# Optimization experiments

Hardware: AMD Instinct MI355X
Metric: run time of the kernel (lower is better)

The kernel has to match this reference:

```python
import jax, jax.numpy as jnp
import numpy as np

NUM_CLASSES = 10
NPTS = 100            # quadrature points per unit interval (torch default npts=100)
EPS = 1e-5            # self.epsilon in the torch module
BATCH = 131072
C_IN = 512


def _betaln(a, b):
    return jax.lax.lgamma(a) + jax.lax.lgamma(b) - jax.lax.lgamma(a + b)


def setup_inputs() -> dict:
    key = jax.random.key(0)
    k1, k2, k3, k4, k5 = jax.random.split(key, 5)
    s = 1.0 / np.sqrt(C_IN).astype(np.float32)
    x = jax.random.normal(k1, (BATCH, C_IN), dtype=jnp.float32)
    W_alpha = jax.random.normal(k2, (C_IN, 1), dtype=jnp.float32) * s
    b_alpha = jax.random.normal(k3, (1,), dtype=jnp.float32) * s
    W_beta = jax.random.normal(k4, (C_IN, 1), dtype=jnp.float32) * s
    b_beta = jax.random.normal(k5, (1,), dtype=jnp.float32) * s
    return {"x": x, "W_alpha": W_alpha, "b_alpha": b_alpha,
            "W_beta": W_beta, "b_beta": b_beta}


def reference(x, W_alpha, b_alpha, W_beta, b_beta):
    # alpha, beta: [B, 1], clamp(1 + softplus(linear(x)), 1, 100)
    alpha = jnp.clip(1.0 + jax.nn.softplus(x @ W_alpha + b_alpha), 1.0, 100.0)
    beta = jnp.clip(1.0 + jax.nn.softplus(x @ W_beta + b_beta), 1.0, 100.0)
    lbeta = _betaln(alpha, beta)  # [B, 1] log Beta-function normalizer
    dx = 1.0 / (NPTS * NUM_CLASSES)

    def unnorm_cdf(b_thr):
        # torch: linspace(eps, b-eps, int(npts*b)); Beta.log_prob broadcast [B, n]
        n = int(NPTS * b_thr)
        if n == 0:
            return jnp.zeros((x.shape[0],), dtype=x.dtype)
        grid = jnp.linspace(EPS, b_thr - EPS, n, dtype=x.dtype)  # [n]
        logpdf = ((alpha - 1.0) * jnp.log(grid)
                  + (beta - 1.0) * jnp.log1p(-grid)
                  - lbeta)  # [B, n]
        return jnp.exp(logpdf).sum(axis=1) * dx  # [B]

    # thresholds i/C for i = 0..C (static Python loop over C+1 small fixed set)
    cdfs = [unnorm_cdf(i / NUM_CLASSES) for i in range(NUM_CLASSES + 1)]
    probs = jnp.stack([cdfs[i + 1] - cdfs[i] for i in range(NUM_CLASSES)], axis=1)  # [B, C]
    # torch uses diag(1/rowsum) @ probs == row-broadcast normalization
    return probs / probs.sum(axis=1, keepdims=True)
```

## Files before the change

### kernel.cpp

```cpp
#include <hip/hip_runtime.h>
#include <math.h>

#define EPS_F 1e-5f
#define NPOINTS 550
#define CIN 512

static __device__ __forceinline__ float softplus_f(float z) {
    return fmaxf(z, 0.0f) + log1pf(expf(-fabsf(z)));
}

static __device__ __forceinline__ float dot8(const float4 a0, const float4 a1,
                                             const float4 w0, const float4 w1) {
    float s = a0.x * w0.x;
    s = fmaf(a0.y, w0.y, s);
    s = fmaf(a0.z, w0.z, s);
    s = fmaf(a0.w, w0.w, s);
    s = fmaf(a1.x, w1.x, s);
    s = fmaf(a1.y, w1.y, s);
    s = fmaf(a1.z, w1.z, s);
    s = fmaf(a1.w, w1.w, s);
    return s;
}

__global__ __launch_bounds__(256, 4) void beta_unimodal_kernel(
    const float* __restrict__ x,
    const float* __restrict__ Wa, const float* __restrict__ ba,
    const float* __restrict__ Wb, const float* __restrict__ bb,
    float* __restrict__ out)
{
    __shared__ float2 tab[NPOINTS];
    __shared__ float outbuf[32 * 10];
    __shared__ float part[4][2][8][68];

    const int tid = threadIdx.x;

    for (int p = tid; p < NPOINTS; p += 256) {
        int i = 1, off = 0;
        while (p >= off + 10 * i) { off += 10 * i; ++i; }
        const int j = p - off;
        const int n = 10 * i;
        const float thr = (float)i * 0.1f;
        const float step = (thr - 2.0f * EPS_F) / (float)(n - 1);
        const float g = EPS_F + step * (float)j;
        float2 e;
        e.x = log2f(g);
        e.y = log2f(1.0f - g);
        tab[p] = e;
    }
    __syncthreads();

    const int lane = tid & 63;
    const int wave = tid >> 6;
    const long rowBase = (long)blockIdx.x * 32 + wave * 8;

    const float4* Wa4 = (const float4*)Wa;
    const float4* Wb4 = (const float4*)Wb;
    const float4 wa0 = Wa4[lane], wa1 = Wa4[64 + lane];
    const float4 wb0 = Wb4[lane], wb1 = Wb4[64 + lane];

    float pa[8], pb[8];
    #pragma unroll
    for (int r = 0; r < 8; ++r) {
        const float4* xr = (const float4*)(x + (rowBase + r) * CIN);
        const float4 x0 = xr[lane];
        const float4 x1 = xr[64 + lane];
        pa[r] = dot8(x0, x1, wa0, wa1);
        pb[r] = dot8(x0, x1, wb0, wb1);
    }

    #pragma unroll
    for (int r = 0; r < 8; ++r) {
        part[wave][0][r][lane] = pa[r];
        part[wave][1][r][lane] = pb[r];
    }
    asm volatile("s_waitcnt lgkmcnt(0)" ::: "memory");

    const int row = lane >> 3;
    const int o = lane & 7;
    const int v = o >> 2;
    const int qa = o & 3;
    const float2* src2 = (const float2*)&part[wave][v][row][qa * 16];
    float s = 0.0f;
    #pragma unroll
    for (int c = 0; c < 8; ++c) {
        const float2 t = src2[c];
        s += t.x + t.y;
    }
    s += __shfl_xor(s, 1, 64);
    s += __shfl_xor(s, 2, 64);
    const float other = __shfl_xor(s, 4, 64);
    const float my_da = (v == 0) ? s : other;
    const float my_db = (v == 0) ? other : s;

    const float za = my_da + ba[0];
    const float zb = my_db + bb[0];
    const float alpha = fminf(fmaxf(1.0f + softplus_f(za), 1.0f), 100.0f);
    const float beta  = fminf(fmaxf(1.0f + softplus_f(zb), 1.0f), 100.0f);
    const float am1 = alpha - 1.0f;
    const float bm1 = beta - 1.0f;

    const float denom = am1 + bm1;
    float mode = (denom > 0.0f) ? (am1 / denom) : 0.5f;
    mode = fminf(fmaxf(mode, 1e-7f), 1.0f - 1.1920929e-7f);
    const float M2 = am1 * log2f(mode) + bm1 * log2f(1.0f - mode);

    float seg[10];
    int p0 = 0;
    #pragma unroll
    for (int i = 1; i <= 10; ++i) {
        const int n = 10 * i;
        float s2 = 0.0f;
        for (int j = o; j < n; j += 8) {
            const float2 t = tab[p0 + j];
            const float e = fmaf(am1, t.x, bm1 * t.y) - M2;
            s2 += __builtin_amdgcn_exp2f(e);
        }
        s2 += __shfl_xor(s2, 1, 64);
        s2 += __shfl_xor(s2, 2, 64);
        s2 += __shfl_xor(s2, 4, 64);
        seg[i - 1] = s2;
        p0 += n;
    }

    const float inv = 1.0f / seg[9];
    const int rowLocal = wave * 8 + row;
    {
        const float prev = (o > 0) ? seg[o - 1] : 0.0f;
        outbuf[rowLocal * 10 + o] = (seg[o] - prev) * inv;
        if (o < 2) {
            const int k = o + 8;
            outbuf[rowLocal * 10 + k] = (seg[k] - seg[k - 1]) * inv;
        }
    }
    __syncthreads();

    if (tid < 80) {
        const float4* src = (const float4*)outbuf;
        float4* dst = (float4*)(out + (size_t)blockIdx.x * 320);
        dst[tid] = src[tid];
    }
}

extern "C" void kernel_launch(void* const* d_in, const int* in_sizes, int n_in,
                              void* d_out, int out_size, void* d_ws, size_t ws_size,
                              hipStream_t stream) {
    const float* x  = (const float*)d_in[0];
    const float* Wa = (const float*)d_in[1];
    const float* ba = (const float*)d_in[2];
    const float* Wb = (const float*)d_in[3];
    const float* bb = (const float*)d_in[4];
    float* out = (float*)d_out;

    const int batch = in_sizes[0] / CIN;
    const int blocks = batch / 32;
    beta_unimodal_kernel<<<blocks, 256, 0, stream>>>(x, Wa, ba, Wb, bb, out);
}
```

Before: 362.3 us.

## Process 64 rows per wave with double-buffered x loads across iterations

Each wave now loops over eight 8-row chunks and prefetches the next chunk of x into registers while computing the current one. The goal is to hide global-load latency and to amortise the per-block log-table setup and weight loads over eight times more rows. The table sum now reads two grid points per float4 from LDS, and outputs are written straight to global memory instead of being staged through shared memory. In exchange, register pressure rises (launch bounds drop to 2 blocks per SIMD), the grid shrinks eightfold, and output stores become less coalesced.

```diff
diff --git a/kernel.cpp b/kernel.cpp
--- a/kernel.cpp
+++ b/kernel.cpp
@@ -4,6 +4,7 @@
 #define EPS_F 1e-5f
 #define NPOINTS 550
 #define CIN 512
+#define NITER 8
 
 static __device__ __forceinline__ float softplus_f(float z) {
     return fmaxf(z, 0.0f) + log1pf(expf(-fabsf(z)));
@@ -22,17 +23,32 @@
     return s;
 }
 
-__global__ __launch_bounds__(256, 4) void beta_unimodal_kernel(
+__global__ __launch_bounds__(256, 2) void beta_unimodal_kernel(
     const float* __restrict__ x,
     const float* __restrict__ Wa, const float* __restrict__ ba,
     const float* __restrict__ Wb, const float* __restrict__ bb,
     float* __restrict__ out)
 {
-    __shared__ float2 tab[NPOINTS];
-    __shared__ float outbuf[32 * 10];
-    __shared__ float part[4][2][8][68];
+    __shared__ __align__(16) float2 tab[NPOINTS];
+    __shared__ float part[4][2][9][68];
 
     const int tid = threadIdx.x;
+    const int lane = tid & 63;
+    const int wave = tid >> 6;
+    const long waveRow0 = ((long)blockIdx.x * 4 + wave) * 64;
+
+    const float4* Wa4 = (const float4*)Wa;
+    const float4* Wb4 = (const float4*)Wb;
+    const float4 wa0 = Wa4[lane], wa1 = Wa4[64 + lane];
+    const float4 wb0 = Wb4[lane], wb1 = Wb4[64 + lane];
+
+    float4 xs[2][8][2];
+    #pragma unroll
+    for (int r = 0; r < 8; ++r) {
+        const float4* xr = (const float4*)(x + (waveRow0 + r) * CIN);
+        xs[0][r][0] = xr[lane];
+        xs[0][r][1] = xr[64 + lane];
+    }
 
     for (int p = tid; p < NPOINTS; p += 256) {
         int i = 1, off = 0;
@@ -49,95 +65,95 @@
     }
     __syncthreads();
 
-    const int lane = tid & 63;
-    const int wave = tid >> 6;
-    const long rowBase = (long)blockIdx.x * 32 + wave * 8;
-
-    const float4* Wa4 = (const float4*)Wa;
-    const float4* Wb4 = (const float4*)Wb;
-    const float4 wa0 = Wa4[lane], wa1 = Wa4[64 + lane];
-    const float4 wb0 = Wb4[lane], wb1 = Wb4[64 + lane];
-
-    float pa[8], pb[8];
-    #pragma unroll
-    for (int r = 0; r < 8; ++r) {
-        const float4* xr = (const float4*)(x + (rowBase + r) * CIN);
-        const float4 x0 = xr[lane];
-        const float4 x1 = xr[64 + lane];
-        pa[r] = dot8(x0, x1, wa0, wa1);
-        pb[r] = dot8(x0, x1, wb0, wb1);
-    }
-
-    #pragma unroll
-    for (int r = 0; r < 8; ++r) {
-        part[wave][0][r][lane] = pa[r];
-        part[wave][1][r][lane] = pb[r];
-    }
-    asm volatile("s_waitcnt lgkmcnt(0)" ::: "memory");
-
+    const float biasA = ba[0], biasB = bb[0];
     const int row = lane >> 3;
     const int o = lane & 7;
     const int v = o >> 2;
     const int qa = o & 3;
-    const float2* src2 = (const float2*)&part[wave][v][row][qa * 16];
-    float s = 0.0f;
+
     #pragma unroll
-    for (int c = 0; c < 8; ++c) {
-        const float2 t = src2[c];
-        s += t.x + t.y;
-    }
-    s += __shfl_xor(s, 1, 64);
-    s += __shfl_xor(s, 2, 64);
-    const float other = __shfl_xor(s, 4, 64);
-    const float my_da = (v == 0) ? s : other;
-    const float my_db = (v == 0) ? other : s;
+    for (int t = 0; t < NITER; ++t) {
+        const int cur = t & 1;
 
-    const float za = my_da + ba[0];
-    const float zb = my_db + bb[0];
-    const float alpha = fminf(fmaxf(1.0f + softplus_f(za), 1.0f), 100.0f);
-    const float beta  = fminf(fmaxf(1.0f + softplus_f(zb), 1.0f), 100.0f);
-    const float am1 = alpha - 1.0f;
-    const float bm1 = beta - 1.0f;
+        if (t + 1 < NITER) {
+            #pragma unroll
+            for (int r = 0; r < 8; ++r) {
+                const float4* xr =
+                    (const float4*)(x + (waveRow0 + (long)(t + 1) * 8 + r) * CIN);
+                xs[cur ^ 1][r][0] = xr[lane];
+                xs[cur ^ 1][r][1] = xr[64 + lane];
+            }
+        }
 
-    const float denom = am1 + bm1;
-    float mode = (denom > 0.0f) ? (am1 / denom) : 0.5f;
-    mode = fminf(fmaxf(mode, 1e-7f), 1.0f - 1.1920929e-7f);
-    const float M2 = am1 * log2f(mode) + bm1 * log2f(1.0f - mode);
+        float pa[8], pb[8];
+        #pragma unroll
+        for (int r = 0; r < 8; ++r) {
+            pa[r] = dot8(xs[cur][r][0], xs[cur][r][1], wa0, wa1);
+            pb[r] = dot8(xs[cur][r][0], xs[cur][r][1], wb0, wb1);
+        }
 
-    float seg[10];
-    int p0 = 0;
-    #pragma unroll
-    for (int i = 1; i <= 10; ++i) {
-        const int n = 10 * i;
-        float s2 = 0.0f;
-        for (int j = o; j < n; j += 8) {
-            const float2 t = tab[p0 + j];
-            const float e = fmaf(am1, t.x, bm1 * t.y) - M2;
-            s2 += __builtin_amdgcn_exp2f(e);
+        #pragma unroll
+        for (int r = 0; r < 8; ++r) {
+            part[wave][0][r][lane] = pa[r];
+            part[wave][1][r][lane] = pb[r];
         }
-        s2 += __shfl_xor(s2, 1, 64);
-        s2 += __shfl_xor(s2, 2, 64);
-        s2 += __shfl_xor(s2, 4, 64);
-        seg[i - 1] = s2;
-        p0 += n;
-    }
+        asm volatile("s_waitcnt lgkmcnt(0)" ::: "memory");
 
-    const float inv = 1.0f / seg[9];
-    const int rowLocal = wave * 8 + row;
-    {
-        const float prev = (o > 0) ? seg[o - 1] : 0.0f;
-        outbuf[rowLocal * 10 + o] = (seg[o] - prev) * inv;
-        if (o < 2) {
-            const int k = o + 8;
-            outbuf[rowLocal * 10 + k] = (seg[k] - seg[k - 1]) * inv;
+        const float4* src4 = (const float4*)&part[wave][v][row][qa * 16];
+        float s = 0.0f;
+        #pragma unroll
+        for (int c = 0; c < 4; ++c) {
+            const float4 tt = src4[c];
+            s += (tt.x + tt.y) + (tt.z + tt.w);
         }
-    }
-    __syncthreads();
+        s += __shfl_xor(s, 1, 64);
+        s += __shfl_xor(s, 2, 64);
+        const float other = __shfl_xor(s, 4, 64);
+        const float my_da = (v == 0) ? s : other;
+        const float my_db = (v == 0) ? other : s;
 
-    if (tid < 80) {
-        const float4* src = (const float4*)outbuf;
-        float4* dst = (float4*)(out + (size_t)blockIdx.x * 320);
-        dst[tid] = src[tid];
+        const float za = my_da + biasA;
+        const float zb = my_db + biasB;
+        const float alpha = fminf(fmaxf(1.0f + softplus_f(za), 1.0f), 100.0f);
+        const float beta  = fminf(fmaxf(1.0f + softplus_f(zb), 1.0f), 100.0f);
+        const float am1 = alpha - 1.0f;
+        const float bm1 = beta - 1.0f;
+
+        const float denom = am1 + bm1;
+        float mode = (denom > 0.0f) ? (am1 / denom) : 0.5f;
+        mode = fminf(fmaxf(mode, 1e-7f), 1.0f - 1.1920929e-7f);
+        const float M2 = am1 * log2f(mode) + bm1 * log2f(1.0f - mode);
+
+        float seg[10];
+        int p0 = 0;
+        #pragma unroll
+        for (int i = 1; i <= 10; ++i) {
+            const int n = 10 * i;
+            float s2 = 0.0f;
+            for (int j2 = 2 * o; j2 < n; j2 += 16) {
+                const float4 tq = *(const float4*)&tab[p0 + j2];
+                const float e0 = fmaf(am1, tq.x, bm1 * tq.y) - M2;
+                const float e1 = fmaf(am1, tq.z, bm1 * tq.w) - M2;
+                s2 += __builtin_amdgcn_exp2f(e0) + __builtin_amdgcn_exp2f(e1);
+            }
+            s2 += __shfl_xor(s2, 1, 64);
+            s2 += __shfl_xor(s2, 2, 64);
+            s2 += __shfl_xor(s2, 4, 64);
+            seg[i - 1] = s2;
+            p0 += n;
+        }
+
+        const float inv = 1.0f / seg[9];
+        float v0 = 0.0f, v1 = 0.0f;
+        #pragma unroll
+        for (int k = 0; k < 10; ++k) {
+            const float pv = (seg[k] - (k ? seg[k - 1] : 0.0f)) * inv;
+            if (k < 8) { if (o == k) v0 = pv; }
+            else       { if (o == k - 8) v1 = pv; }
+        }
+        float* orow = out + (waveRow0 + (long)t * 8 + row) * 10;
+        orow[o] = v0;
+        if (o < 2) orow[8 + o] = v1;
     }
 }
 
@@ -152,6 +168,6 @@
     float* out = (float*)d_out;
 
     const int batch = in_sizes[0] / CIN;
-    const int blocks = batch / 32;
+    const int blocks = batch / (4 * 64);
     beta_unimodal_kernel<<<blocks, 256, 0, stream>>>(x, Wa, ba, Wb, bb, out);
 }
```

New measurement: 376.9 us. 1.04x slower.
